# Optimization experiments

Measured on AMD Instinct MI355X. Metric: run time of the kernel, lower is better.

The kernel has to match this reference:

```python
import math
import jax, jax.numpy as jnp
import numpy as np

D = 128
R = 64
BETA = 1.0


def setup_inputs() -> dict:
    key = jax.random.key(0)
    k1, k2 = jax.random.split(key)
    X_tilde = jax.random.normal(k1, (8, 2048, D), dtype=jnp.float32)
    W = jax.random.normal(k2, (D, R), dtype=jnp.float32) / math.sqrt(R)
    return {"X_tilde": X_tilde, "W": W}


def reference(X_tilde, W):
    # S = W W^T / sqrt(d*r), shape (d, d)
    d, r = W.shape
    S = (W @ W.T) / math.sqrt(d * r)
    B, T, _ = X_tilde.shape
    # gram = X S X^T, shape (B, T, T)
    XS = jnp.einsum('btd,de->bte', X_tilde, S)
    gram = jnp.einsum('bte,bse->bts', XS, X_tilde)
    # trace-centering: subtract (tr(gram)/T) * I
    trace = jnp.einsum('btt->b', gram)  # (B,)
    eye = jnp.eye(T, dtype=X_tilde.dtype)
    centered = gram - (trace / T)[:, None, None] * eye[None, :, :]
    scores = centered / math.sqrt(d)  # normalize_sqrt_d=True
    A = jax.nn.softmax(BETA * scores, axis=-1)  # (B, T, T)
    Y_hat = jnp.einsum('bts,bsd->btd', A, X_tilde)
    return Y_hat
```

## Files before the change

kernel.cpp:

```cpp
#include <hip/hip_runtime.h>
#include <hip/hip_bf16.h>
#include <math.h>

#define D_DIM 128
#define R_DIM 64
#define T_DIM 2048
#define B_DIM 8
#define NS 4
#define SCHUNK (T_DIM / NS)
#define SBLK 32
#define NIT (SCHUNK / SBLK)
#define KE_CONST (0.08838834764831845f * 1.4426950408889634f)

typedef __attribute__((ext_vector_type(8))) short bf16x8;
typedef __attribute__((ext_vector_type(4))) short s16x4;
typedef __attribute__((ext_vector_type(4))) float f32x4;
typedef __attribute__((ext_vector_type(16))) float f32x16;

__device__ inline unsigned short f2bf(float f) {
  union { float f; unsigned int u; } v; v.f = f;
  return (unsigned short)((v.u + 0x7FFFu + ((v.u >> 16) & 1u)) >> 16);
}
__device__ inline float bf2f(unsigned short u) {
  union { unsigned int u; float f; } v; v.u = ((unsigned int)u) << 16;
  return v.f;
}
__device__ inline unsigned int cvt_pk_bf16(float lo, float hi) {
  unsigned int r;
  asm("v_cvt_pk_bf16_f32 %0, %1, %2" : "=v"(r) : "v"(lo), "v"(hi));
  return r;
}
__device__ inline void permswap(unsigned int& a, unsigned int& b) {
  asm("v_permlane32_swap_b32 %0, %1" : "+v"(a), "+v"(b));
}

__device__ inline void async16(const short* l, const unsigned short* g) {
  __builtin_amdgcn_global_load_lds(
      (const __attribute__((address_space(1))) unsigned int*)g,
      (__attribute__((address_space(3))) unsigned int*)l, 16, 0, 0);
}

__global__ void k_s(const float* __restrict__ W, unsigned short* __restrict__ Sb) {
  int gid = blockIdx.x * 256 + threadIdx.x;
  int i = gid >> 7, j = gid & 127;
  const float* wi = W + i * R_DIM;
  const float* wj = W + j * R_DIM;
  float acc = 0.f;
#pragma unroll 8
  for (int r = 0; r < R_DIM; ++r) acc += wi[r] * wj[r];
  Sb[gid] = f2bf(acc * 0.011048543456039806f);
}

__global__ void __launch_bounds__(128) k_prep(
    const float* __restrict__ X, const unsigned short* __restrict__ Sb,
    unsigned short* __restrict__ Qb, unsigned short* __restrict__ Xb,
    unsigned short* __restrict__ Xt, float* __restrict__ part) {
  const int tid = threadIdx.x;
  const int w = tid >> 6, lane = tid & 63;
  const int g = lane >> 4, c = lane & 15;
  const int b = blockIdx.y;
  const int t0 = blockIdx.x * 32;
  const int tw = t0 + w * 16;

  __shared__ __align__(16) short xbT[D_DIM * 32];
  __shared__ float red[2];

  union FU { unsigned int wd[4]; bf16x8 v; };
  bf16x8 xf[4];
#pragma unroll
  for (int kc = 0; kc < 4; ++kc) {
    const float* xp = X + ((size_t)(b * T_DIM + tw + c)) * D_DIM + kc * 32 + g * 8;
    f32x4 a = *(const f32x4*)xp;
    f32x4 bb = *(const f32x4*)(xp + 4);
    FU f;
    f.wd[0] = cvt_pk_bf16(a[0], a[1]);
    f.wd[1] = cvt_pk_bf16(a[2], a[3]);
    f.wd[2] = cvt_pk_bf16(bb[0], bb[1]);
    f.wd[3] = cvt_pk_bf16(bb[2], bb[3]);
    xf[kc] = f.v;
    *(bf16x8*)(Xb + ((size_t)(b * T_DIM + tw + c)) * D_DIM + kc * 32 + g * 8) = f.v;
#pragma unroll
    for (int jw = 0; jw < 4; ++jw) {
      unsigned int wv = f.wd[jw];
      int e = kc * 32 + g * 8 + jw * 2;
      xbT[(e + 0) * 32 + w * 16 + c] = (short)wv;
      xbT[(e + 1) * 32 + w * 16 + c] = (short)(wv >> 16);
    }
  }

  f32x4 acc[8];
#pragma unroll
  for (int dc = 0; dc < 8; ++dc) acc[dc] = (f32x4){0.f, 0.f, 0.f, 0.f};
#pragma unroll
  for (int dc = 0; dc < 8; ++dc) {
    bf16x8 sf[4];
#pragma unroll
    for (int kc = 0; kc < 4; ++kc)
      sf[kc] = *(const bf16x8*)(Sb + (size_t)(dc * 16 + c) * D_DIM + kc * 32 + g * 8);
#pragma unroll
    for (int kc = 0; kc < 4; ++kc)
      acc[dc] = __builtin_amdgcn_mfma_f32_16x16x32_bf16(xf[kc], sf[kc], acc[dc], 0, 0, 0);
  }

  __syncthreads();

  float trp = 0.f;
#pragma unroll
  for (int dc = 0; dc < 8; ++dc)
#pragma unroll
    for (int r = 0; r < 4; ++r) {
      float q = acc[dc][r];
      float x = bf2f((unsigned short)xbT[(dc * 16 + c) * 32 + w * 16 + g * 4 + r]);
      trp += q * x;
      unsigned int pk = cvt_pk_bf16(q * KE_CONST, 0.f);
      Qb[((size_t)(b * T_DIM + tw + g * 4 + r)) * D_DIM + dc * 16 + c] = (unsigned short)pk;
    }

#pragma unroll
  for (int p = 0; p < 4; ++p) {
    int row = p * 32 + (tid >> 2);
    bf16x8 v = *(const bf16x8*)&xbT[row * 32 + (tid & 3) * 8];
    *(bf16x8*)(Xt + ((size_t)(b * D_DIM + row)) * T_DIM + t0 + (tid & 3) * 8) = v;
  }

  trp += __shfl_xor(trp, 1); trp += __shfl_xor(trp, 2);
  trp += __shfl_xor(trp, 4); trp += __shfl_xor(trp, 8);
  trp += __shfl_xor(trp, 16); trp += __shfl_xor(trp, 32);
  if (lane == 0) red[w] = trp;
  __syncthreads();
  if (tid == 0) part[b * 64 + blockIdx.x] = red[0] + red[1];
}

__global__ void __launch_bounds__(256, 2) k_attn(
    const unsigned short* __restrict__ Qb, const unsigned short* __restrict__ Xb,
    const unsigned short* __restrict__ Xt, const float* __restrict__ part,
    unsigned short* __restrict__ accp, float* __restrict__ rsp) {
  const int tid = threadIdx.x;
  const int wave = tid >> 6, lane = tid & 63;
  const int tl = lane & 31;
  const int h = lane >> 5;
  const int lin = blockIdx.x;
  const int b = lin & 7;
  const int kk = lin >> 3;
  const int ns = kk & 3;
  const int t0w = (kk >> 2) * 128 + wave * 32;

  const unsigned short* Qbb = Qb + (size_t)b * T_DIM * D_DIM;
  const unsigned short* Xbb = Xb + (size_t)b * T_DIM * D_DIM;
  const unsigned short* Xtb = Xt + (size_t)b * D_DIM * T_DIM;

  float tv = part[b * 64 + lane];
  tv += __shfl_xor(tv, 1); tv += __shfl_xor(tv, 2);
  tv += __shfl_xor(tv, 4); tv += __shfl_xor(tv, 8);
  tv += __shfl_xor(tv, 16); tv += __shfl_xor(tv, 32);
  const float ctrK = tv * (1.0f / T_DIM) * KE_CONST;

  __shared__ __align__(16) short sKs[2][SBLK * D_DIM];
  __shared__ __align__(16) short sVs[2][D_DIM * SBLK];

  int oK[8], oV[4][2];
#pragma unroll
  for (int kc = 0; kc < 8; ++kc)
    oK[kc] = tl * 128 + (((kc * 2 + h) ^ (tl & 15)) * 8);
#pragma unroll
  for (int dt = 0; dt < 4; ++dt)
#pragma unroll
    for (int sck = 0; sck < 2; ++sck)
      oV[dt][sck] = (dt * 32 + tl) * 32 + (((sck * 2 + h) ^ (tl & 3)) * 8);

  bf16x8 qf[8];
#pragma unroll
  for (int kc = 0; kc < 8; ++kc)
    qf[kc] = *(const bf16x8*)(Qbb + (size_t)(t0w + tl) * D_DIM + kc * 16 + h * 8);

  f32x16 acc[4];
#pragma unroll
  for (int dt = 0; dt < 4; ++dt)
#pragma unroll
    for (int r = 0; r < 16; ++r) acc[dt][r] = 0.f;
  float denacc = 0.f;

  const int s_beg = ns * SCHUNK;

  auto stage = [&](int buf, int sb) {
#pragma unroll
    for (int q = 0; q < 2; ++q) {
      int j = wave * 128 + q * 64 + lane;
      int row = j >> 4, sc = j & 15;
      int lc = sc ^ (row & 15);
      async16(&sKs[buf][(wave * 128 + q * 64) * 8],
              Xbb + (size_t)(sb + row) * D_DIM + lc * 8);
    }
#pragma unroll
    for (int q = 0; q < 2; ++q) {
      int j = wave * 128 + q * 64 + lane;
      int row = j >> 2, sc = j & 3;
      int lc = sc ^ (row & 3);
      async16(&sVs[buf][(wave * 128 + q * 64) * 8],
              Xtb + (size_t)row * T_DIM + sb + lc * 8);
    }
  };

  stage(0, s_beg);
  __syncthreads();

  for (int it = 0; it < NIT; ++it) {
    const int buf = it & 1;
    const int sb = s_beg + it * SBLK;
    if (it < NIT - 1) stage(buf ^ 1, sb + SBLK);

    const short* kb = &sKs[buf][0];
    const short* vb = &sVs[buf][0];

    bf16x8 kf[8];
#pragma unroll
    for (int kc = 0; kc < 8; ++kc)
      kf[kc] = *(const bf16x8*)(kb + oK[kc]);
    bf16x8 vf[4][2];
#pragma unroll
    for (int dt = 0; dt < 4; ++dt)
#pragma unroll
      for (int sck = 0; sck < 2; ++sck)
        vf[dt][sck] = *(const bf16x8*)(vb + oV[dt][sck]);

    f32x16 sc;
#pragma unroll
    for (int r = 0; r < 16; ++r) sc[r] = 0.f;
#pragma unroll
    for (int kc = 0; kc < 8; ++kc)
      sc = __builtin_amdgcn_mfma_f32_32x32x16_bf16(kf[kc], qf[kc], sc, 0, 0, 0);

    const bool isd = (sb == t0w);

#pragma unroll
    for (int sck = 0; sck < 2; ++sck) {
      float p[8];
#pragma unroll
      for (int q = 0; q < 8; ++q) {
        int rowid = (q & 3) + 8 * (q >> 2) + 16 * sck + 4 * h;
        float v = sc[sck * 8 + q];
        if (isd && rowid == tl) v -= ctrK;
        p[q] = exp2f(v);
        denacc += p[q];
      }
      unsigned int W0 = cvt_pk_bf16(p[0], p[1]);
      unsigned int W1 = cvt_pk_bf16(p[2], p[3]);
      unsigned int W2 = cvt_pk_bf16(p[4], p[5]);
      unsigned int W3 = cvt_pk_bf16(p[6], p[7]);
      permswap(W0, W2);
      permswap(W1, W3);
      union PU { unsigned int wd[4]; bf16x8 v; } pu;
      pu.wd[0] = W0; pu.wd[1] = W1; pu.wd[2] = W2; pu.wd[3] = W3;
#pragma unroll
      for (int dt = 0; dt < 4; ++dt)
        acc[dt] = __builtin_amdgcn_mfma_f32_32x32x16_bf16(pu.v, vf[dt][sck],
                                                          acc[dt], 0, 0, 0);
    }

    __syncthreads();
  }

  float den = denacc + __shfl_xor(denacc, 32);
  if (lane < 32)
    rsp[(b * NS + ns) * T_DIM + t0w + lane] = den;

  const size_t pbase = ((size_t)(b * NS + ns)) * T_DIM * D_DIM;
#pragma unroll
  for (int dt = 0; dt < 4; ++dt)
#pragma unroll
    for (int r = 0; r < 16; ++r) {
      int rowid = (r & 3) + 8 * (r >> 2) + 4 * h;
      accp[pbase + (size_t)(t0w + rowid) * D_DIM + dt * 32 + tl] =
          (unsigned short)cvt_pk_bf16(acc[dt][r], 0.f);
    }
}

__global__ void __launch_bounds__(256) k_comb(
    const unsigned short* __restrict__ accp, const float* __restrict__ rsp,
    float* __restrict__ out) {
  const int lin = blockIdx.x;
  const int b = lin & 7;
  const int kk = lin >> 3;
  int ib = kk * 1024 + threadIdx.x * 4;
  int d = ib & 127;
  int t = ib >> 7;
  float num0 = 0.f, num1 = 0.f, num2 = 0.f, num3 = 0.f, den = 0.f;
#pragma unroll
  for (int ns = 0; ns < NS; ++ns) {
    const unsigned short* p =
        accp + (((size_t)(b * NS + ns)) * T_DIM + t) * D_DIM + d;
    s16x4 v = *(const s16x4*)p;
    num0 += bf2f((unsigned short)v[0]);
    num1 += bf2f((unsigned short)v[1]);
    num2 += bf2f((unsigned short)v[2]);
    num3 += bf2f((unsigned short)v[3]);
    den += rsp[(b * NS + ns) * T_DIM + t];
  }
  float inv = 1.0f / den;
  f32x4 o = (f32x4){num0 * inv, num1 * inv, num2 * inv, num3 * inv};
  *(f32x4*)(out + ((size_t)b * T_DIM * D_DIM + ib)) = o;
}

extern "C" void kernel_launch(void* const* d_in, const int* in_sizes, int n_in,
                              void* d_out, int out_size, void* d_ws, size_t ws_size,
                              hipStream_t stream) {
  const float* X = (const float*)d_in[0];
  const float* W = (const float*)d_in[1];
  float* out = (float*)d_out;
  char* ws = (char*)d_ws;

  unsigned short* Sb = (unsigned short*)(ws);
  float* part        = (float*)(ws + 32768);
  unsigned short* Qb = (unsigned short*)(ws + 65536);
  unsigned short* Xb = (unsigned short*)(ws + 65536 + 4194304);
  unsigned short* Xt = (unsigned short*)(ws + 65536 + 2 * 4194304);
  unsigned short* accp = (unsigned short*)(ws + 65536 + 3 * 4194304);
  float* rsp         = (float*)(ws + 65536 + 3 * 4194304 + 16777216);

  k_s<<<64, 256, 0, stream>>>(W, Sb);
  k_prep<<<dim3(T_DIM / 32, B_DIM), 128, 0, stream>>>(X, Sb, Qb, Xb, Xt, part);
  k_attn<<<(T_DIM / 128) * NS * B_DIM, 256, 0, stream>>>(Qb, Xb, Xt, part, accp, rsp);
  k_comb<<<B_DIM * 256, 256, 0, stream>>>(accp, rsp, out);
}
```

Baseline: 50.89 us.

## Process two query tiles per wave in attention and pre-swizzle Q/S layouts

Each attention wave now handles 64 query rows as two 32-row tiles that share each staged K/V block, so LDS fragment loads are reused across twice the work. Grid size is halved and launch bounds drop to one block per CU to make room for the doubled accumulator registers. Q and S are written in MFMA-fragment-friendly swizzled layouts so they can be loaded with contiguous per-lane vector reads. The trade-off is lower occupancy and fewer blocks (256) across the device, which reduces latency hiding and load balance.

```diff
diff --git a/kernel.cpp b/kernel.cpp
--- a/kernel.cpp
+++ b/kernel.cpp
@@ -48,7 +48,8 @@
   float acc = 0.f;
 #pragma unroll 8
   for (int r = 0; r < R_DIM; ++r) acc += wi[r] * wj[r];
-  Sb[gid] = f2bf(acc * 0.011048543456039806f);
+  int off = (((i >> 4) * 4 + (j >> 5)) * 64 + ((j & 31) >> 3) * 16 + (i & 15)) * 8 + (j & 7);
+  Sb[off] = f2bf(acc * 0.011048543456039806f);
 }
 
 __global__ void __launch_bounds__(128) k_prep(
@@ -96,7 +97,7 @@
     bf16x8 sf[4];
 #pragma unroll
     for (int kc = 0; kc < 4; ++kc)
-      sf[kc] = *(const bf16x8*)(Sb + (size_t)(dc * 16 + c) * D_DIM + kc * 32 + g * 8);
+      sf[kc] = *(const bf16x8*)(Sb + ((size_t)(dc * 4 + kc) * 64 + lane) * 8);
 #pragma unroll
     for (int kc = 0; kc < 4; ++kc)
       acc[dc] = __builtin_amdgcn_mfma_f32_16x16x32_bf16(xf[kc], sf[kc], acc[dc], 0, 0, 0);
@@ -112,8 +113,10 @@
       float q = acc[dc][r];
       float x = bf2f((unsigned short)xbT[(dc * 16 + c) * 32 + w * 16 + g * 4 + r]);
       trp += q * x;
-      unsigned int pk = cvt_pk_bf16(q * KE_CONST, 0.f);
-      Qb[((size_t)(b * T_DIM + tw + g * 4 + r)) * D_DIM + dc * 16 + c] = (unsigned short)pk;
+      int t = tw + g * 4 + r;
+      size_t qoff = (((size_t)(b * 64 + (t >> 5)) * 8 + dc) * 512 +
+                     ((c >> 3) * 32 + (t & 31)) * 8 + (c & 7));
+      Qb[qoff] = (unsigned short)cvt_pk_bf16(q * KE_CONST, 0.f);
     }
 
 #pragma unroll
@@ -131,7 +134,7 @@
   if (tid == 0) part[b * 64 + blockIdx.x] = red[0] + red[1];
 }
 
-__global__ void __launch_bounds__(256, 2) k_attn(
+__global__ void __launch_bounds__(256, 1) k_attn(
     const unsigned short* __restrict__ Qb, const unsigned short* __restrict__ Xb,
     const unsigned short* __restrict__ Xt, const float* __restrict__ part,
     unsigned short* __restrict__ accp, float* __restrict__ rsp) {
@@ -143,9 +146,9 @@
   const int b = lin & 7;
   const int kk = lin >> 3;
   const int ns = kk & 3;
-  const int t0w = (kk >> 2) * 128 + wave * 32;
-
-  const unsigned short* Qbb = Qb + (size_t)b * T_DIM * D_DIM;
+  const int tile = kk >> 2;
+  const int t0w = tile * 256 + wave * 64;
+
   const unsigned short* Xbb = Xb + (size_t)b * T_DIM * D_DIM;
   const unsigned short* Xtb = Xt + (size_t)b * D_DIM * T_DIM;
 
@@ -168,17 +171,21 @@
     for (int sck = 0; sck < 2; ++sck)
       oV[dt][sck] = (dt * 32 + tl) * 32 + (((sck * 2 + h) ^ (tl & 3)) * 8);
 
-  bf16x8 qf[8];
-#pragma unroll
-  for (int kc = 0; kc < 8; ++kc)
-    qf[kc] = *(const bf16x8*)(Qbb + (size_t)(t0w + tl) * D_DIM + kc * 16 + h * 8);
-
-  f32x16 acc[4];
+  const unsigned short* qbase =
+      Qb + ((size_t)(b * 64 + tile * 8 + wave * 2)) * 8 * 512;
+  bf16x8 qf0[8], qf1[8];
+#pragma unroll
+  for (int kc = 0; kc < 8; ++kc) {
+    qf0[kc] = *(const bf16x8*)(qbase + (size_t)kc * 512 + lane * 8);
+    qf1[kc] = *(const bf16x8*)(qbase + (size_t)(8 + kc) * 512 + lane * 8);
+  }
+
+  f32x16 acc0[4], acc1[4];
 #pragma unroll
   for (int dt = 0; dt < 4; ++dt)
 #pragma unroll
-    for (int r = 0; r < 16; ++r) acc[dt][r] = 0.f;
-  float denacc = 0.f;
+    for (int r = 0; r < 16; ++r) { acc0[dt][r] = 0.f; acc1[dt][r] = 0.f; }
+  float den0 = 0.f, den1 = 0.f;
 
   const int s_beg = ns * SCHUNK;
 
@@ -223,46 +230,82 @@
       for (int sck = 0; sck < 2; ++sck)
         vf[dt][sck] = *(const bf16x8*)(vb + oV[dt][sck]);
 
-    f32x16 sc;
-#pragma unroll
-    for (int r = 0; r < 16; ++r) sc[r] = 0.f;
-#pragma unroll
-    for (int kc = 0; kc < 8; ++kc)
-      sc = __builtin_amdgcn_mfma_f32_32x32x16_bf16(kf[kc], qf[kc], sc, 0, 0, 0);
-
-    const bool isd = (sb == t0w);
-
-#pragma unroll
-    for (int sck = 0; sck < 2; ++sck) {
-      float p[8];
-#pragma unroll
-      for (int q = 0; q < 8; ++q) {
-        int rowid = (q & 3) + 8 * (q >> 2) + 16 * sck + 4 * h;
-        float v = sc[sck * 8 + q];
-        if (isd && rowid == tl) v -= ctrK;
-        p[q] = exp2f(v);
-        denacc += p[q];
+    {
+      f32x16 sc;
+#pragma unroll
+      for (int r = 0; r < 16; ++r) sc[r] = 0.f;
+#pragma unroll
+      for (int kc = 0; kc < 8; ++kc)
+        sc = __builtin_amdgcn_mfma_f32_32x32x16_bf16(kf[kc], qf0[kc], sc, 0, 0, 0);
+      const bool isd = (sb == t0w);
+#pragma unroll
+      for (int sck = 0; sck < 2; ++sck) {
+        float p[8];
+#pragma unroll
+        for (int q = 0; q < 8; ++q) {
+          int rowid = (q & 3) + 8 * (q >> 2) + 16 * sck + 4 * h;
+          float v = sc[sck * 8 + q];
+          if (isd && rowid == tl) v -= ctrK;
+          p[q] = exp2f(v);
+          den0 += p[q];
+        }
+        unsigned int W0 = cvt_pk_bf16(p[0], p[1]);
+        unsigned int W1 = cvt_pk_bf16(p[2], p[3]);
+        unsigned int W2 = cvt_pk_bf16(p[4], p[5]);
+        unsigned int W3 = cvt_pk_bf16(p[6], p[7]);
+        permswap(W0, W2);
+        permswap(W1, W3);
+        union PU { unsigned int wd[4]; bf16x8 v; } pu;
+        pu.wd[0] = W0; pu.wd[1] = W1; pu.wd[2] = W2; pu.wd[3] = W3;
+#pragma unroll
+        for (int dt = 0; dt < 4; ++dt)
+          acc0[dt] = __builtin_amdgcn_mfma_f32_32x32x16_bf16(pu.v, vf[dt][sck],
+                                                             acc0[dt], 0, 0, 0);
       }
-      unsigned int W0 = cvt_pk_bf16(p[0], p[1]);
-      unsigned int W1 = cvt_pk_bf16(p[2], p[3]);
-      unsigned int W2 = cvt_pk_bf16(p[4], p[5]);
-      unsigned int W3 = cvt_pk_bf16(p[6], p[7]);
-      permswap(W0, W2);
-      permswap(W1, W3);
-      union PU { unsigned int wd[4]; bf16x8 v; } pu;
-      pu.wd[0] = W0; pu.wd[1] = W1; pu.wd[2] = W2; pu.wd[3] = W3;
-#pragma unroll
-      for (int dt = 0; dt < 4; ++dt)
-        acc[dt] = __builtin_amdgcn_mfma_f32_32x32x16_bf16(pu.v, vf[dt][sck],
-                                                          acc[dt], 0, 0, 0);
+    }
+    {
+      f32x16 sc;
+#pragma unroll
+      for (int r = 0; r < 16; ++r) sc[r] = 0.f;
+#pragma unroll
+      for (int kc = 0; kc < 8; ++kc)
+        sc = __builtin_amdgcn_mfma_f32_32x32x16_bf16(kf[kc], qf1[kc], sc, 0, 0, 0);
+      const bool isd = (sb == t0w + 32);
+#pragma unroll
+      for (int sck = 0; sck < 2; ++sck) {
+        float p[8];
+#pragma unroll
+        for (int q = 0; q < 8; ++q) {
+          int rowid = (q & 3) + 8 * (q >> 2) + 16 * sck + 4 * h;
+          float v = sc[sck * 8 + q];
+          if (isd && rowid == tl) v -= ctrK;
+          p[q] = exp2f(v);
+          den1 += p[q];
+        }
+        unsigned int W0 = cvt_pk_bf16(p[0], p[1]);
+        unsigned int W1 = cvt_pk_bf16(p[2], p[3]);
+        unsigned int W2 = cvt_pk_bf16(p[4], p[5]);
+        unsigned int W3 = cvt_pk_bf16(p[6], p[7]);
+        permswap(W0, W2);
+        permswap(W1, W3);
+        union PU { unsigned int wd[4]; bf16x8 v; } pu;
+        pu.wd[0] = W0; pu.wd[1] = W1; pu.wd[2] = W2; pu.wd[3] = W3;
+#pragma unroll
+        for (int dt = 0; dt < 4; ++dt)
+          acc1[dt] = __builtin_amdgcn_mfma_f32_32x32x16_bf16(pu.v, vf[dt][sck],
+                                                             acc1[dt], 0, 0, 0);
+      }
     }
 
     __syncthreads();
   }
 
-  float den = denacc + __shfl_xor(denacc, 32);
-  if (lane < 32)
-    rsp[(b * NS + ns) * T_DIM + t0w + lane] = den;
+  float d0 = den0 + __shfl_xor(den0, 32);
+  float d1 = den1 + __shfl_xor(den1, 32);
+  if (lane < 32) {
+    rsp[(b * NS + ns) * T_DIM + t0w + lane] = d0;
+    rsp[(b * NS + ns) * T_DIM + t0w + 32 + lane] = d1;
+  }
 
   const size_t pbase = ((size_t)(b * NS + ns)) * T_DIM * D_DIM;
 #pragma unroll
@@ -271,7 +314,9 @@
     for (int r = 0; r < 16; ++r) {
       int rowid = (r & 3) + 8 * (r >> 2) + 4 * h;
       accp[pbase + (size_t)(t0w + rowid) * D_DIM + dt * 32 + tl] =
-          (unsigned short)cvt_pk_bf16(acc[dt][r], 0.f);
+          (unsigned short)cvt_pk_bf16(acc0[dt][r], 0.f);
+      accp[pbase + (size_t)(t0w + 32 + rowid) * D_DIM + dt * 32 + tl] =
+          (unsigned short)cvt_pk_bf16(acc1[dt][r], 0.f);
     }
 }
 
@@ -319,6 +364,6 @@
 
   k_s<<<64, 256, 0, stream>>>(W, Sb);
   k_prep<<<dim3(T_DIM / 32, B_DIM), 128, 0, stream>>>(X, Sb, Qb, Xb, Xt, part);
-  k_attn<<<(T_DIM / 128) * NS * B_DIM, 256, 0, stream>>>(Qb, Xb, Xt, part, accp, rsp);
+  k_attn<<<(T_DIM / 256) * NS * B_DIM, 256, 0, stream>>>(Qb, Xb, Xt, part, accp, rsp);
   k_comb<<<B_DIM * 256, 256, 0, stream>>>(accp, rsp, out);
 }
```

Measured after the change: 56.13 us. 10.3% more time.

## Pre-swizzle S and Q into MFMA fragment order and overlap staging loads

Applied to the files above, without the earlier changes.

S and Q are written in MFMA-fragment-contiguous layouts so the consumer kernels load each operand as one coalesced 16-byte-per-lane read. In the attention loop, the full __syncthreads after each stage is replaced by a partial vmcnt wait plus a raw s_barrier. This lets the next tile's global-to-LDS loads stay in flight while the current tile is computed. The hand-written waitcnt and barrier ordering depends on the exact count of outstanding loads, so it risks races if the compiler reorders or adds memory ops.

```diff
diff --git a/kernel.cpp b/kernel.cpp
--- a/kernel.cpp
+++ b/kernel.cpp
@@ -48,7 +48,8 @@
   float acc = 0.f;
 #pragma unroll 8
   for (int r = 0; r < R_DIM; ++r) acc += wi[r] * wj[r];
-  Sb[gid] = f2bf(acc * 0.011048543456039806f);
+  int off = (((i >> 4) * 4 + (j >> 5)) * 64 + ((j & 31) >> 3) * 16 + (i & 15)) * 8 + (j & 7);
+  Sb[off] = f2bf(acc * 0.011048543456039806f);
 }
 
 __global__ void __launch_bounds__(128) k_prep(
@@ -96,7 +97,7 @@
     bf16x8 sf[4];
 #pragma unroll
     for (int kc = 0; kc < 4; ++kc)
-      sf[kc] = *(const bf16x8*)(Sb + (size_t)(dc * 16 + c) * D_DIM + kc * 32 + g * 8);
+      sf[kc] = *(const bf16x8*)(Sb + ((size_t)(dc * 4 + kc) * 64 + lane) * 8);
 #pragma unroll
     for (int kc = 0; kc < 4; ++kc)
       acc[dc] = __builtin_amdgcn_mfma_f32_16x16x32_bf16(xf[kc], sf[kc], acc[dc], 0, 0, 0);
@@ -112,8 +113,10 @@
       float q = acc[dc][r];
       float x = bf2f((unsigned short)xbT[(dc * 16 + c) * 32 + w * 16 + g * 4 + r]);
       trp += q * x;
-      unsigned int pk = cvt_pk_bf16(q * KE_CONST, 0.f);
-      Qb[((size_t)(b * T_DIM + tw + g * 4 + r)) * D_DIM + dc * 16 + c] = (unsigned short)pk;
+      int t = tw + g * 4 + r;
+      size_t qoff = (((size_t)(b * 64 + (t >> 5)) * 8 + dc) * 512 +
+                     ((c >> 3) * 32 + (t & 31)) * 8 + (c & 7));
+      Qb[qoff] = (unsigned short)cvt_pk_bf16(q * KE_CONST, 0.f);
     }
 
 #pragma unroll
@@ -143,9 +146,9 @@
   const int b = lin & 7;
   const int kk = lin >> 3;
   const int ns = kk & 3;
-  const int t0w = (kk >> 2) * 128 + wave * 32;
-
-  const unsigned short* Qbb = Qb + (size_t)b * T_DIM * D_DIM;
+  const int tile = kk >> 2;
+  const int t0w = tile * 128 + wave * 32;
+
   const unsigned short* Xbb = Xb + (size_t)b * T_DIM * D_DIM;
   const unsigned short* Xtb = Xt + (size_t)b * D_DIM * T_DIM;
 
@@ -168,10 +171,12 @@
     for (int sck = 0; sck < 2; ++sck)
       oV[dt][sck] = (dt * 32 + tl) * 32 + (((sck * 2 + h) ^ (tl & 3)) * 8);
 
+  const unsigned short* qbase =
+      Qb + ((size_t)(b * 64 + tile * 4 + wave)) * 8 * 512;
   bf16x8 qf[8];
 #pragma unroll
   for (int kc = 0; kc < 8; ++kc)
-    qf[kc] = *(const bf16x8*)(Qbb + (size_t)(t0w + tl) * D_DIM + kc * 16 + h * 8);
+    qf[kc] = *(const bf16x8*)(qbase + (size_t)kc * 512 + lane * 8);
 
   f32x16 acc[4];
 #pragma unroll
@@ -202,12 +207,19 @@
   };
 
   stage(0, s_beg);
-  __syncthreads();
 
   for (int it = 0; it < NIT; ++it) {
     const int buf = it & 1;
     const int sb = s_beg + it * SBLK;
-    if (it < NIT - 1) stage(buf ^ 1, sb + SBLK);
+
+    if (it < NIT - 1) {
+      stage(buf ^ 1, sb + SBLK);
+      asm volatile("s_waitcnt vmcnt(4)" ::: "memory");
+    } else {
+      asm volatile("s_waitcnt vmcnt(0)" ::: "memory");
+    }
+    __builtin_amdgcn_sched_barrier(0);
+    __builtin_amdgcn_s_barrier();
 
     const short* kb = &sKs[buf][0];
     const short* vb = &sVs[buf][0];
@@ -257,7 +269,7 @@
                                                           acc[dt], 0, 0, 0);
     }
 
-    __syncthreads();
+    __builtin_amdgcn_s_barrier();
   }
 
   float den = denacc + __shfl_xor(denacc, 32);
```

Result: faster. 46.21 us (-9.2%).
